# Performance work log

Hardware: AMD Instinct MI355X
Metric: run time of the kernel (lower is better)

## Reference

```python
import jax, jax.numpy as jnp
import numpy as np

DEPTH = 4
HEADS = 8
DIM = 512
DH = DIM // HEADS          # 64
M_FEAT = 256               # FAVOR+ random features
FF = 4 * DIM               # 2048
EPS_K = 1e-4               # FAVOR+ stabilizer
LN_EPS = 1e-5


def _gorf(rng, m, d):
    # gaussian orthogonal random features (lucidrains default, scaling=0)
    blocks = []
    for _ in range(m // d):
        g = rng.normal(size=(d, d))
        q, _ = np.linalg.qr(g)
        blocks.append(q.T)
    Q = np.concatenate(blocks, axis=0)[:m]
    mult = np.linalg.norm(rng.normal(size=(m, d)), axis=1)
    return (mult[:, None] * Q).astype(np.float32)


def setup_inputs() -> dict:
    rng = np.random.default_rng(0)
    B, T, L = 2, 8, 512
    s = 0.02
    x = rng.normal(size=(B, T, L, DIM)).astype(np.float32)
    proj = np.stack([_gorf(rng, M_FEAT, DH) for _ in range(DEPTH)])  # [depth, m, dh]
    def w(*shape):
        return (rng.normal(size=shape) * s).astype(np.float32)
    inp = {
        "x": jnp.asarray(x),
        "proj": jnp.asarray(proj),
        "ln1_g": jnp.ones((DEPTH, DIM), jnp.float32),
        "ln1_b": jnp.zeros((DEPTH, DIM), jnp.float32),
        "Wqkv": jnp.asarray(w(DEPTH, DIM, 3 * DIM)),
        "bqkv": jnp.zeros((DEPTH, 3 * DIM), jnp.float32),
        "Wo": jnp.asarray(w(DEPTH, DIM, DIM)),
        "bo": jnp.zeros((DEPTH, DIM), jnp.float32),
        "ln2_g": jnp.ones((DEPTH, DIM), jnp.float32),
        "ln2_b": jnp.zeros((DEPTH, DIM), jnp.float32),
        "Wff1": jnp.asarray(w(DEPTH, DIM, FF)),
        "bff1": jnp.zeros((DEPTH, FF), jnp.float32),
        "Wff2": jnp.asarray(w(DEPTH, FF, DIM)),
        "bff2": jnp.zeros((DEPTH, DIM), jnp.float32),
    }
    return inp


def _layer_norm(x, g, b):
    mu = jnp.mean(x, -1, keepdims=True)
    var = jnp.mean(jnp.square(x - mu), -1, keepdims=True)
    return (x - mu) * jax.lax.rsqrt(var + LN_EPS) * g + b


def _softmax_kernel(data, proj, is_query):
    # FAVOR+ positive softmax-kernel features (Performer)
    dh = data.shape[-1]
    dn = dh ** -0.25                       # data normalizer
    ratio = proj.shape[0] ** -0.5
    dd = jnp.einsum("bhnd,md->bhnm", data, proj) * dn
    diag = jnp.sum(jnp.square(data), -1, keepdims=True) * (0.5 * dn * dn)
    if is_query:
        mx = jnp.max(dd, axis=-1, keepdims=True)
    else:
        mx = jnp.max(dd, axis=(-1, -2), keepdims=True)
    return ratio * (jnp.exp(dd - diag - mx) + EPS_K)


def _attention(x, Wqkv, bqkv, Wo, bo, proj):
    B, N, D = x.shape
    qkv = x @ Wqkv + bqkv                                   # [B,N,3D]
    q, k, v = jnp.split(qkv, 3, axis=-1)
    def heads(t):
        return t.reshape(B, N, HEADS, DH).transpose(0, 2, 1, 3)  # [B,H,N,dh]
    q, k, v = heads(q), heads(k), heads(v)
    qp = _softmax_kernel(q, proj, True)                     # [B,H,N,m]
    kp = _softmax_kernel(k, proj, False)
    k_sum = jnp.sum(kp, axis=-2)                            # [B,H,m]
    d_inv = 1.0 / jnp.einsum("bhnm,bhm->bhn", qp, k_sum)
    ctx = jnp.einsum("bhnm,bhnd->bhmd", kp, v)              # [B,H,m,dh]
    out = jnp.einsum("bhmd,bhnm,bhn->bhnd", ctx, qp, d_inv)
    out = out.transpose(0, 2, 1, 3).reshape(B, N, D)
    return out @ Wo + bo


def reference(x, proj, ln1_g, ln1_b, Wqkv, bqkv, Wo, bo, ln2_g, ln2_b, Wff1, bff1, Wff2, bff2):
    B, T, L, D = x.shape
    h = x.reshape(B, T * L, D)
    for i in range(DEPTH):
        a = _attention(_layer_norm(h, ln1_g[i], ln1_b[i]), Wqkv[i], bqkv[i], Wo[i], bo[i], proj[i])
        h = h + a
        f = _layer_norm(h, ln2_g[i], ln2_b[i])
        f = jax.nn.gelu(f @ Wff1[i] + bff1[i], approximate=False) @ Wff2[i] + bff2[i]
        h = h + f
    return h.reshape(B, T, L, D)
```

## Files before the change

kernel.cpp:

```cpp
#include <hip/hip_runtime.h>
#include <math.h>

#define DEPTH 4
#define DMODEL 512
#define DH 64
#define MF 256
#define FFD 2048
#define SEQN 4096
#define NROWS 8192

typedef __bf16 bf16_t;
typedef bf16_t bf16x8 __attribute__((ext_vector_type(8)));
typedef bf16_t bf16x4 __attribute__((ext_vector_type(4)));
typedef bf16_t bf16x2 __attribute__((ext_vector_type(2)));
typedef float f32x4v __attribute__((ext_vector_type(4)));

static constexpr float DN = 0.35355339059327373f;
static constexpr float RATIO = 0.0625f;
static constexpr float EPSK = 1e-4f;

__device__ __forceinline__ float gelu_fast(float x) {
    float z2 = x * (1.5957691216f + 0.0713548162f * x * x);
    return x / (1.0f + __expf(-z2));
}

#define AS1(p) ((const __attribute__((address_space(1))) void*)(p))
#define AS3(p) ((__attribute__((address_space(3))) void*)(p))

template <int N> __device__ __forceinline__ void wait_vmcnt() {
    if constexpr (N == 0) asm volatile("s_waitcnt vmcnt(0)" ::: "memory");
    else if constexpr (N == 1) asm volatile("s_waitcnt vmcnt(1)" ::: "memory");
    else if constexpr (N == 2) asm volatile("s_waitcnt vmcnt(2)" ::: "memory");
    else if constexpr (N == 3) asm volatile("s_waitcnt vmcnt(3)" ::: "memory");
    else if constexpr (N == 4) asm volatile("s_waitcnt vmcnt(4)" ::: "memory");
    else if constexpr (N == 5) asm volatile("s_waitcnt vmcnt(5)" ::: "memory");
    else if constexpr (N == 6) asm volatile("s_waitcnt vmcnt(6)" ::: "memory");
    else if constexpr (N == 8) asm volatile("s_waitcnt vmcnt(8)" ::: "memory");
    else asm volatile("s_waitcnt vmcnt(12)" ::: "memory");
}

__global__ __launch_bounds__(256) void ln_kernel(const float* __restrict__ h,
                                                 const float* __restrict__ g,
                                                 const float* __restrict__ b,
                                                 bf16_t* __restrict__ y) {
    int row = blockIdx.x, tid = threadIdx.x;
    const float* hr = h + (size_t)row * DMODEL;
    float v0 = hr[tid], v1 = hr[tid + 256];
    __shared__ float s_sum[256], s_sq[256];
    s_sum[tid] = v0 + v1;
    s_sq[tid] = v0 * v0 + v1 * v1;
    __syncthreads();
    for (int off = 128; off > 0; off >>= 1) {
        if (tid < off) { s_sum[tid] += s_sum[tid + off]; s_sq[tid] += s_sq[tid + off]; }
        __syncthreads();
    }
    float mu = s_sum[0] * (1.0f / DMODEL);
    float var = s_sq[0] * (1.0f / DMODEL) - mu * mu;
    float rstd = rsqrtf(var + 1e-5f);
    bf16_t* yr = y + (size_t)row * DMODEL;
    yr[tid]       = (bf16_t)((v0 - mu) * rstd * g[tid] + b[tid]);
    yr[tid + 256] = (bf16_t)((v1 - mu) * rstd * g[tid + 256] + b[tid + 256]);
}

__global__ __launch_bounds__(256) void ln_add_kernel(const float* __restrict__ hin,
                                                     float* __restrict__ hout,
                                                     const bf16_t* __restrict__ p,
                                                     const float* __restrict__ g,
                                                     const float* __restrict__ b,
                                                     bf16_t* __restrict__ y) {
    int row = blockIdx.x, tid = threadIdx.x;
    const float* hr = hin + (size_t)row * DMODEL;
    const bf16_t* pr = p + (size_t)row * DMODEL;
    float2 hv = *(const float2*)(hr + 2 * tid);
    bf16x2 pv = *(const bf16x2*)(pr + 2 * tid);
    float v0 = hv.x + (float)pv[0];
    float v1 = hv.y + (float)pv[1];
    float2 outv; outv.x = v0; outv.y = v1;
    *(float2*)(hout + (size_t)row * DMODEL + 2 * tid) = outv;
    __shared__ float s_sum[256], s_sq[256];
    s_sum[tid] = v0 + v1;
    s_sq[tid] = v0 * v0 + v1 * v1;
    __syncthreads();
    for (int off = 128; off > 0; off >>= 1) {
        if (tid < off) { s_sum[tid] += s_sum[tid + off]; s_sq[tid] += s_sq[tid + off]; }
        __syncthreads();
    }
    float mu = s_sum[0] * (1.0f / DMODEL);
    float var = s_sq[0] * (1.0f / DMODEL) - mu * mu;
    float rstd = rsqrtf(var + 1e-5f);
    bf16x2 ov;
    ov[0] = (bf16_t)((v0 - mu) * rstd * g[2 * tid] + b[2 * tid]);
    ov[1] = (bf16_t)((v1 - mu) * rstd * g[2 * tid + 1] + b[2 * tid + 1]);
    *(bf16x2*)(y + (size_t)row * DMODEL + 2 * tid) = ov;
}

__global__ __launch_bounds__(256) void add_kernel(float* __restrict__ h,
                                                  const bf16_t* __restrict__ p) {
    size_t i = ((size_t)blockIdx.x * 256 + threadIdx.x) * 4;
    float4 hv = *(const float4*)(h + i);
    bf16x4 pv = *(const bf16x4*)(p + i);
    hv.x += (float)pv[0]; hv.y += (float)pv[1];
    hv.z += (float)pv[2]; hv.w += (float)pv[3];
    *(float4*)(h + i) = hv;
}

__global__ __launch_bounds__(256) void wconv_all(const float* __restrict__ Wqkv,
                                                 const float* __restrict__ Wo,
                                                 const float* __restrict__ Wff1,
                                                 const float* __restrict__ Wff2,
                                                 bf16_t* __restrict__ wslot) {
    __shared__ float t[32][33];
    int layer = blockIdx.y;
    int bid = blockIdx.x;
    const float* W; bf16_t* Wt; int K, N, nx, lb;
    bf16_t* slot = wslot + (size_t)layer * 3407872;
    if (bid < 768)       { W = Wqkv + (size_t)layer * 786432;  Wt = slot;           K = 512;  N = 1536; nx = 48; lb = bid; }
    else if (bid < 1024) { W = Wo   + (size_t)layer * 262144;  Wt = slot + 786432;  K = 512;  N = 512;  nx = 16; lb = bid - 768; }
    else if (bid < 2048) { W = Wff1 + (size_t)layer * 1048576; Wt = slot + 1048576; K = 512;  N = 2048; nx = 64; lb = bid - 1024; }
    else                 { W = Wff2 + (size_t)layer * 1048576; Wt = slot + 2097152; K = 2048; N = 512;  nx = 16; lb = bid - 2048; }
    int n0 = (lb % nx) * 32, k0 = (lb / nx) * 32;
    int tx = threadIdx.x & 31, ty = threadIdx.x >> 5;
#pragma unroll
    for (int i = 0; i < 32; i += 8)
        t[ty + i][tx] = W[(size_t)(k0 + ty + i) * N + n0 + tx];
    __syncthreads();
#pragma unroll
    for (int i = 0; i < 32; i += 8)
        Wt[(size_t)(n0 + ty + i) * K + k0 + tx] = (bf16_t)t[tx][ty + i];
}

__global__ __launch_bounds__(256) void pconv_kernel(const float* __restrict__ proj,
                                                    bf16_t* __restrict__ projb) {
    int i = (blockIdx.x * 256 + threadIdx.x) * 4;
    float4 v = *(const float4*)(proj + i);
    bf16x4 o;
    o[0] = (bf16_t)v.x; o[1] = (bf16_t)v.y; o[2] = (bf16_t)v.z; o[3] = (bf16_t)v.w;
    *(bf16x4*)(projb + i) = o;
}

template <int BM, int BN, int BK, int P, int ACT, int RES, int WF, int WB, int QKVE>
__global__ __launch_bounds__(256) void gemm_pipe(const bf16_t* __restrict__ A,
                                                 const bf16_t* __restrict__ Bt,
                                                 const float* __restrict__ bias,
                                                 float* __restrict__ Cf,
                                                 bf16_t* __restrict__ Cb,
                                                 bf16_t* __restrict__ Vt,
                                                 int N, int K) {
    static_assert(BK == 32, "BK fixed at 32 (KS==1)");
    constexpr int MR = BM / 2 / 16;
    constexpr int NR = BN / 2 / 16;
    constexpr int CH = BK / 8;
    constexpr int SWZ = CH - 1;
    constexpr int TILE = (BM + BN) * BK;
    constexpr int L = TILE / 8 / 256;
    __shared__ __attribute__((aligned(16))) bf16_t smem[P * TILE];
    int tid = threadIdx.x;
    int wv = tid >> 6, ln = tid & 63;
    int gx = gridDim.x;
    int lin = blockIdx.y * gx + blockIdx.x;
    int per = (gx * gridDim.y) >> 3;
    int orig = (lin & 7) * per + (lin >> 3);
    int m0 = (orig / gx) * BM, n0 = (orig % gx) * BN;
    int wr = (wv >> 1) * (MR * 16), wc = (wv & 1) * (NR * 16);
    int lr = ln & 15, kq8 = ln >> 4;
    int nsteps = K / BK;

    const bf16_t* gsrc[L];
    int ldst[L];
#pragma unroll
    for (int i = 0; i < L; i++) {
        int c = i * 256 + tid;
        int cb = i * 256 + (tid & ~63);
        bool inA = (c < BM * CH);
        int cc = inA ? c : c - BM * CH;
        int row = cc / CH, ch = cc % CH;
        const bf16_t* mat = inA ? A : Bt;
        int r0 = inA ? m0 : n0;
        int chs = ch ^ ((row ^ (row >> 2)) & SWZ);
        gsrc[i] = mat + (size_t)(r0 + row) * K + chs * 8;
        ldst[i] = cb * 8;
    }
    auto stage = [&](int tile, int sb) {
        int k0 = tile * BK;
        bf16_t* dst = smem + sb * TILE;
#pragma unroll
        for (int i = 0; i < L; i++)
            __builtin_amdgcn_global_load_lds(AS1(gsrc[i] + k0), AS3(dst + ldst[i]), 16, 0, 0);
    };

    int aoff[MR], boff[NR];
#pragma unroll
    for (int m = 0; m < MR; m++) {
        int row = wr + m * 16 + lr;
        aoff[m] = (row * CH + (kq8 ^ ((row ^ (row >> 2)) & SWZ))) * 8;
    }
#pragma unroll
    for (int n = 0; n < NR; n++) {
        int row = wc + n * 16 + lr;
        boff[n] = BM * BK + (row * CH + (kq8 ^ ((row ^ (row >> 2)) & SWZ))) * 8;
    }

    f32x4v acc[MR][NR] = {};
#pragma unroll
    for (int p = 0; p < P - 1; ++p) stage(p, p);

    int cur = 0;
    for (int t = 0; t < nsteps; ++t) {
        int rem = nsteps - 1 - t;
        if (rem >= P - 2) wait_vmcnt<(P - 2) * L>();
        else if constexpr (P >= 4) {
            if (rem == 1) wait_vmcnt<L>(); else wait_vmcnt<0>();
        } else wait_vmcnt<0>();
        __builtin_amdgcn_s_barrier();
        asm volatile("" ::: "memory");
        if (t + P - 1 < nsteps) {
            int sb = cur - 1; if (sb < 0) sb = P - 1;
            stage(t + P - 1, sb);
        }
        const bf16_t* base = smem + cur * TILE;
        bf16x8 af[MR], bfr[NR];
#pragma unroll
        for (int m = 0; m < MR; m++) af[m] = *(const bf16x8*)&base[aoff[m]];
#pragma unroll
        for (int n = 0; n < NR; n++) bfr[n] = *(const bf16x8*)&base[boff[n]];
        __builtin_amdgcn_s_setprio(1);
#pragma unroll
        for (int m = 0; m < MR; m++)
#pragma unroll
            for (int n = 0; n < NR; n++)
                acc[m][n] = __builtin_amdgcn_mfma_f32_16x16x32_bf16(af[m], bfr[n], acc[m][n], 0, 0, 0);
        __builtin_amdgcn_s_setprio(0);
        cur = (cur + 1 == P) ? 0 : cur + 1;
    }
    int rq = (ln >> 4) * 4;
    if (WB || QKVE) {
        __syncthreads();
        bf16_t* T = smem;
        constexpr int S = BN + 8;
#pragma unroll
        for (int n = 0; n < NR; n++) {
            int col = wc + n * 16 + lr;
            float bcol = bias[n0 + col];
#pragma unroll
            for (int m = 0; m < MR; m++) {
#pragma unroll
                for (int r = 0; r < 4; r++) {
                    int row = wr + m * 16 + rq + r;
                    float v = acc[m][n][r] + bcol;
                    if (ACT == 1) v = gelu_fast(v);
                    int cs = (col & 7) | ((((col >> 3) ^ (row >> 3)) & (BN / 8 - 1)) << 3);
                    T[row * S + cs] = (bf16_t)v;
                }
            }
        }
        __syncthreads();
        if (!QKVE || n0 < 1024) {
            int ldc = QKVE ? 1024 : N;
#pragma unroll
            for (int i = 0; i < BM * BN / 8 / 256; i++) {
                int e = i * 2048 + tid * 8;
                int row = e / BN, c0 = e % BN;
                int ch = ((c0 >> 3) ^ (row >> 3)) & (BN / 8 - 1);
                bf16x8 v = *(const bf16x8*)&T[row * S + ch * 8];
                *(bf16x8*)&Cb[(size_t)(m0 + row) * ldc + n0 + c0] = v;
            }
        } else {
#pragma unroll
            for (int i = 0; i < BM * BN / 8 / 256; i++) {
                int u = i * 256 + tid;
                int d = u & (BN - 1), nb8 = (u / BN) * 8;
                bf16x8 v;
#pragma unroll
                for (int j = 0; j < 8; j++) {
                    int row = nb8 + j;
                    int cs = (d & 7) | ((((d >> 3) ^ (row >> 3)) & (BN / 8 - 1)) << 3);
                    v[j] = T[row * S + cs];
                }
                int gcol = n0 + d;
                int hh2 = (gcol >> 6) & 7, dd2 = gcol & 63;
                int grow = m0 + nb8;
                int bb = grow >> 12, nn = grow & 4095;
                *(bf16x8*)&Vt[(((size_t)bb * 8 + hh2) * 64 + dd2) * 4096 + nn] = v;
            }
        }
    } else {
#pragma unroll
        for (int n = 0; n < NR; n++) {
            int col = n0 + wc + n * 16 + lr;
            float bcol = bias[col];
#pragma unroll
            for (int m = 0; m < MR; m++) {
#pragma unroll
                for (int r = 0; r < 4; r++) {
                    int row = m0 + wr + m * 16 + rq + r;
                    float v = acc[m][n][r] + bcol;
                    if (ACT == 1) v = gelu_fast(v);
                    size_t idx = (size_t)row * N + col;
                    if (RES) Cf[idx] += v;
                    else Cf[idx] = v;
                }
            }
        }
    }
}

__global__ __launch_bounds__(256) void feat_kernel(const bf16_t* __restrict__ qkvb,
                                                   const bf16_t* __restrict__ projb,
                                                   bf16_t* __restrict__ outp,
                                                   float* __restrict__ ksum_part) {
    int bid = blockIdx.x;
    int bh = bid >> 5, tile = bid & 31;
    int b = bh >> 3, hh = bh & 7;
    int tid = threadIdx.x, wv = tid >> 6, ln = tid & 63;
    __shared__ __attribute__((aligned(16))) bf16_t AsBs[128 * 64 + 256 * 64];
    bf16_t* As = AsBs;
    bf16_t* Bs = AsBs + 128 * 64;
    __shared__ float diag_s[128];
    __shared__ float ksp_s[256];
    int n0 = tile * 128;
    int qoff = 512 + hh * 64;
    int lrow8 = ln >> 3;
    int lchunk = ((ln & 7) ^ (lrow8 & 7)) * 8;
#pragma unroll
    for (int i = 0; i < 4; i++) {
        int e = wv * 4 + i;
        size_t src = (size_t)(b * SEQN + n0 + e * 8 + lrow8) * 1024 + qoff + lchunk;
        __builtin_amdgcn_global_load_lds(AS1(qkvb + src), AS3(&As[e * 512]), 16, 0, 0);
    }
#pragma unroll
    for (int i = 0; i < 8; i++) {
        int e = wv * 8 + i;
        size_t src = (size_t)(e * 8 + lrow8) * 64 + lchunk;
        __builtin_amdgcn_global_load_lds(AS1(projb + src), AS3(&Bs[e * 512]), 16, 0, 0);
    }
    __syncthreads();
    if (tid < 128) {
        float s = 0.f;
#pragma unroll
        for (int c = 0; c < 8; c++) {
            bf16x8 v = *(const bf16x8*)&As[tid * 64 + ((c ^ (tid & 7)) * 8)];
#pragma unroll
            for (int j = 0; j < 8; j++) { float f = (float)v[j]; s += f * f; }
        }
        diag_s[tid] = s * (0.5f * DN * DN);
    }
    int wr = (wv >> 1) * 64, wc = (wv & 1) * 128;
    int lr = ln & 15, kg = ln >> 4, rq = kg * 4;
    f32x4v acc[4][8] = {};
#pragma unroll
    for (int ks = 0; ks < 2; ks++) {
        int g = ks * 4 + kg;
        bf16x8 af[4], bfv[8];
#pragma unroll
        for (int m = 0; m < 4; m++) {
            int row = wr + m * 16 + lr;
            af[m] = *(const bf16x8*)&As[row * 64 + ((g ^ (row & 7)) * 8)];
        }
#pragma unroll
        for (int n = 0; n < 8; n++) {
            int row = wc + n * 16 + lr;
            bfv[n] = *(const bf16x8*)&Bs[row * 64 + ((g ^ (row & 7)) * 8)];
        }
#pragma unroll
        for (int m = 0; m < 4; m++)
#pragma unroll
            for (int n = 0; n < 8; n++)
                acc[m][n] = __builtin_amdgcn_mfma_f32_16x16x32_bf16(af[m], bfv[n], acc[m][n], 0, 0, 0);
    }
    __syncthreads();
    float sj[8] = {};
#pragma unroll
    for (int m = 0; m < 4; m++) {
#pragma unroll
        for (int n = 0; n < 8; n++) {
#pragma unroll
            for (int r = 0; r < 4; r++) {
                int row = wr + m * 16 + rq + r;
                float val = RATIO * (__expf(acc[m][n][r] * DN - diag_s[row]) + EPSK);
                acc[m][n][r] = val;
                sj[n] += val;
            }
        }
    }
#pragma unroll
    for (int n = 0; n < 8; n++) {
        sj[n] += __shfl_xor(sj[n], 16);
        sj[n] += __shfl_xor(sj[n], 32);
    }
    if (wv < 2 && ln < 16) {
#pragma unroll
        for (int n = 0; n < 8; n++) ksp_s[wc + n * 16 + ln] = sj[n];
    }
    __syncthreads();
    if (wv >= 2 && ln < 16) {
#pragma unroll
        for (int n = 0; n < 8; n++) ksp_s[wc + n * 16 + ln] += sj[n];
    }
    __syncthreads();
    ksum_part[(size_t)bid * 256 + tid] = ksp_s[tid];
    bf16_t* T = AsBs;
#pragma unroll
    for (int hf = 0; hf < 2; hf++) {
        if ((wv & 1) == hf) {
#pragma unroll
            for (int n = 0; n < 8; n++) {
                int mm = n * 16 + lr;
#pragma unroll
                for (int m = 0; m < 4; m++) {
                    int nnb = wr + m * 16 + rq;
                    bf16x4 v;
#pragma unroll
                    for (int r = 0; r < 4; r++) v[r] = (bf16_t)acc[m][n][r];
                    *(bf16x4*)&T[mm * 136 + nnb] = v;
                }
            }
        }
        __syncthreads();
#pragma unroll
        for (int i = 0; i < 8; i++) {
            int u = i * 256 + tid;
            int mm = u >> 4, nc = u & 15;
            bf16x8 v = *(const bf16x8*)&T[mm * 136 + nc * 8];
            *(bf16x8*)&outp[((size_t)bh * MF + hf * 128 + mm) * 4096 + n0 + nc * 8] = v;
        }
        __syncthreads();
    }
}

__global__ __launch_bounds__(256) void ctx_gemm(const bf16_t* __restrict__ KPt,
                                                const bf16_t* __restrict__ Vt,
                                                float* __restrict__ part) {
    int bh = blockIdx.y;
    int mtile = blockIdx.x & 1, kc = blockIdx.x >> 1;
    int m0 = mtile * 128, nb = kc * 512;
    int tid = threadIdx.x, wv = tid >> 6, ln = tid & 63;
    __shared__ __attribute__((aligned(16))) bf16_t As[128 * 64];
    __shared__ __attribute__((aligned(16))) bf16_t Bs[64 * 64];
    int lrow8 = ln >> 3;
    int lchunk = ((ln & 7) ^ (lrow8 & 7)) * 8;
    int lr = ln & 15, kg = ln >> 4, rq = kg * 4;
    int wr = wv * 32;
    f32x4v acc[2][4] = {};
    for (int kt = 0; kt < 8; kt++) {
        int noff = nb + kt * 64;
        __syncthreads();
#pragma unroll
        for (int i = 0; i < 4; i++) {
            int e = wv * 4 + i;
            __builtin_amdgcn_global_load_lds(
                AS1(KPt + ((size_t)bh * MF + m0 + e * 8 + lrow8) * 4096 + noff + lchunk),
                AS3(&As[e * 512]), 16, 0, 0);
        }
#pragma unroll
        for (int i = 0; i < 2; i++) {
            int e = wv * 2 + i;
            __builtin_amdgcn_global_load_lds(
                AS1(Vt + ((size_t)bh * 64 + e * 8 + lrow8) * 4096 + noff + lchunk),
                AS3(&Bs[e * 512]), 16, 0, 0);
        }
        __syncthreads();
#pragma unroll
        for (int ks = 0; ks < 2; ks++) {
            int g = ks * 4 + kg;
            bf16x8 af[2], bfv[4];
#pragma unroll
            for (int m = 0; m < 2; m++) {
                int row = wr + m * 16 + lr;
                af[m] = *(const bf16x8*)&As[row * 64 + ((g ^ (row & 7)) * 8)];
            }
#pragma unroll
            for (int n = 0; n < 4; n++) {
                int row = n * 16 + lr;
                bfv[n] = *(const bf16x8*)&Bs[row * 64 + ((g ^ (row & 7)) * 8)];
            }
#pragma unroll
            for (int m = 0; m < 2; m++)
#pragma unroll
                for (int n = 0; n < 4; n++)
                    acc[m][n] = __builtin_amdgcn_mfma_f32_16x16x32_bf16(af[m], bfv[n], acc[m][n], 0, 0, 0);
        }
    }
#pragma unroll
    for (int m = 0; m < 2; m++)
#pragma unroll
        for (int n = 0; n < 4; n++)
#pragma unroll
            for (int r = 0; r < 4; r++)
                part[((size_t)(kc * 16 + bh) * MF + m0 + wr + m * 16 + rq + r) * 64 + n * 16 + lr] =
                    acc[m][n][r];
}

__global__ __launch_bounds__(256) void ctx_reduce_kernel(const float* __restrict__ part,
                                                         const float* __restrict__ ksum_part,
                                                         bf16_t* __restrict__ ctx_t,
                                                         float* __restrict__ ksum) {
    int bh = blockIdx.x >> 4;
    int chunk = blockIdx.x & 15;
    for (int it = 0; it < 4; it++) {
        int idx = (chunk * 4 + it) * 256 + threadIdx.x;
        int m = idx >> 6, d = idx & 63;
        float s = 0.f;
#pragma unroll
        for (int kc = 0; kc < 8; kc++)
            s += part[(size_t)(kc * 16 + bh) * 16384 + idx];
        ctx_t[((size_t)bh * 64 + d) * MF + m] = (bf16_t)s;
    }
    if (chunk == 0) {
        float s = 0.f;
#pragma unroll
        for (int t = 0; t < 32; t++)
            s += ksum_part[((size_t)bh * 32 + t) * 256 + threadIdx.x];
        ksum[bh * MF + threadIdx.x] = s;
    }
}

__global__ __launch_bounds__(256) void qfused_kernel(const bf16_t* __restrict__ qkvb,
                                                     const bf16_t* __restrict__ projb,
                                                     const bf16_t* __restrict__ ctx_t,
                                                     const float* __restrict__ ksumb,
                                                     bf16_t* __restrict__ abuf) {
    int bid = blockIdx.x;
    int bh = bid >> 5, tile = bid & 31;
    int b = bh >> 3, hh = bh & 7;
    int tid = threadIdx.x, wv = tid >> 6, ln = tid & 63;
    __shared__ __attribute__((aligned(16))) bf16_t Qs[128 * 64];
    __shared__ __attribute__((aligned(16))) bf16_t Ps[256 * 64];
    __shared__ __attribute__((aligned(16))) bf16_t Cs[64 * 256];
    __shared__ float diag_s[128];
    __shared__ float dsum_s[128];
    int n0 = tile * 128;
    int lrow8 = ln >> 3;
    int lchunk = ((ln & 7) ^ (lrow8 & 7)) * 8;
#pragma unroll
    for (int i = 0; i < 4; i++) {
        int e = wv * 4 + i;
        size_t src = (size_t)(b * SEQN + n0 + e * 8 + lrow8) * 1024 + hh * 64 + lchunk;
        __builtin_amdgcn_global_load_lds(AS1(qkvb + src), AS3(&Qs[e * 512]), 16, 0, 0);
    }
#pragma unroll
    for (int i = 0; i < 8; i++) {
        int e = wv * 8 + i;
        size_t src = (size_t)(e * 8 + lrow8) * 64 + lchunk;
        __builtin_amdgcn_global_load_lds(AS1(projb + src), AS3(&Ps[e * 512]), 16, 0, 0);
    }
#pragma unroll
    for (int i = 0; i < 8; i++) {
        int c = i * 256 + tid;
        int cb = i * 256 + (tid & ~63);
        int crow = c >> 5, cch = c & 31;
        size_t src = ((size_t)bh * 64 + crow) * 256 + (size_t)(cch ^ (crow & 7)) * 8;
        __builtin_amdgcn_global_load_lds(AS1(ctx_t + src), AS3(Cs + (size_t)cb * 8), 16, 0, 0);
    }
    int wr = (wv >> 1) * 64, wc = (wv & 1) * 128;
    int lr = ln & 15, kg = ln >> 4, rq = kg * 4;
    float ksum_r[8];
#pragma unroll
    for (int n = 0; n < 8; n++) ksum_r[n] = ksumb[bh * MF + wc + n * 16 + lr];
    __syncthreads();
    if (tid < 128) {
        float s = 0.f;
#pragma unroll
        for (int c = 0; c < 8; c++) {
            bf16x8 v = *(const bf16x8*)&Qs[tid * 64 + ((c ^ (tid & 7)) * 8)];
#pragma unroll
            for (int j = 0; j < 8; j++) { float f = (float)v[j]; s += f * f; }
        }
        diag_s[tid] = s * (0.5f * DN * DN);
    }
    f32x4v acc[4][8] = {};
#pragma unroll
    for (int ks = 0; ks < 2; ks++) {
        int g = ks * 4 + kg;
        bf16x8 af[4], bfv[8];
#pragma unroll
        for (int m = 0; m < 4; m++) {
            int row = wr + m * 16 + lr;
            af[m] = *(const bf16x8*)&Qs[row * 64 + ((g ^ (row & 7)) * 8)];
        }
#pragma unroll
        for (int n = 0; n < 8; n++) {
            int row = wc + n * 16 + lr;
            bfv[n] = *(const bf16x8*)&Ps[row * 64 + ((g ^ (row & 7)) * 8)];
        }
#pragma unroll
        for (int m = 0; m < 4; m++)
#pragma unroll
            for (int n = 0; n < 8; n++)
                acc[m][n] = __builtin_amdgcn_mfma_f32_16x16x32_bf16(af[m], bfv[n], acc[m][n], 0, 0, 0);
    }
    __syncthreads();
    float dsum_p[4][4];
#pragma unroll
    for (int m = 0; m < 4; m++) {
#pragma unroll
        for (int r = 0; r < 4; r++) {
            int row = wr + m * 16 + rq + r;
            float dg = diag_s[row];
            float ds = 0.f;
#pragma unroll
            for (int n = 0; n < 8; n++) {
                float val = RATIO * (__expf(acc[m][n][r] * DN - dg) + EPSK);
                acc[m][n][r] = val;
                ds += val * ksum_r[n];
            }
            dsum_p[m][r] = ds;
        }
    }
#pragma unroll
    for (int m = 0; m < 4; m++)
#pragma unroll
        for (int r = 0; r < 4; r++) {
#pragma unroll
            for (int mask = 1; mask < 16; mask <<= 1)
                dsum_p[m][r] += __shfl_xor(dsum_p[m][r], mask);
        }
    if ((wv & 1) == 0 && lr == 0) {
#pragma unroll
        for (int m = 0; m < 4; m++)
#pragma unroll
            for (int r = 0; r < 4; r++)
                dsum_s[wr + m * 16 + rq + r] = dsum_p[m][r];
    }
    __syncthreads();
    if ((wv & 1) == 1 && lr == 0) {
#pragma unroll
        for (int m = 0; m < 4; m++)
#pragma unroll
            for (int r = 0; r < 4; r++) {
                int row = wr + m * 16 + rq + r;
                dsum_s[row] = 1.0f / (dsum_s[row] + dsum_p[m][r]);
            }
    }
    __syncthreads();
    f32x4v acc_o[4][2] = {};
#pragma unroll
    for (int h = 0; h < 2; h++) {
        if ((wv & 1) == h) {
#pragma unroll
            for (int m = 0; m < 4; m++)
#pragma unroll
                for (int n = 0; n < 8; n++)
#pragma unroll
                    for (int r = 0; r < 4; r++) {
                        int row = wr + m * 16 + rq + r;
                        int ml = n * 16 + lr;
                        Ps[row * 128 + (((ml >> 3) ^ (row & 7)) * 8) + (ml & 7)] =
                            (bf16_t)acc[m][n][r];
                    }
        }
        __syncthreads();
#pragma unroll
        for (int ku = 0; ku < 4; ku++) {
            int g = ku * 4 + kg;
            bf16x8 af[4], bfv[2];
#pragma unroll
            for (int m = 0; m < 4; m++) {
                int row = wr + m * 16 + lr;
                af[m] = *(const bf16x8*)&Ps[row * 128 + ((g ^ (row & 7)) * 8)];
            }
#pragma unroll
            for (int n = 0; n < 2; n++) {
                int rowd = (wv & 1) * 32 + n * 16 + lr;
                int ch = (h * 16 + g) ^ (rowd & 7);
                bfv[n] = *(const bf16x8*)&Cs[(rowd * 32 + ch) * 8];
            }
#pragma unroll
            for (int m = 0; m < 4; m++)
#pragma unroll
                for (int n = 0; n < 2; n++)
                    acc_o[m][n] = __builtin_amdgcn_mfma_f32_16x16x32_bf16(af[m], bfv[n], acc_o[m][n], 0, 0, 0);
        }
        __syncthreads();
    }
#pragma unroll
    for (int m = 0; m < 4; m++) {
#pragma unroll
        for (int r = 0; r < 4; r++) {
            int rowl = wr + m * 16 + rq + r;
            float di = dsum_s[rowl];
            size_t obase = ((size_t)(b * SEQN + n0 + rowl)) * DMODEL + hh * 64;
#pragma unroll
            for (int n = 0; n < 2; n++) {
                int d = (wv & 1) * 32 + n * 16 + lr;
                abuf[obase + d] = (bf16_t)(acc_o[m][n][r] * di);
            }
        }
    }
}

extern "C" void kernel_launch(void* const* d_in, const int* in_sizes, int n_in,
                              void* d_out, int out_size, void* d_ws, size_t ws_size,
                              hipStream_t stream) {
    const float* x     = (const float*)d_in[0];
    const float* proj  = (const float*)d_in[1];
    const float* ln1_g = (const float*)d_in[2];
    const float* ln1_b = (const float*)d_in[3];
    const float* Wqkv  = (const float*)d_in[4];
    const float* bqkv  = (const float*)d_in[5];
    const float* Wo    = (const float*)d_in[6];
    const float* bo    = (const float*)d_in[7];
    const float* ln2_g = (const float*)d_in[8];
    const float* ln2_b = (const float*)d_in[9];
    const float* Wff1  = (const float*)d_in[10];
    const float* bff1  = (const float*)d_in[11];
    const float* Wff2  = (const float*)d_in[12];
    const float* bff2  = (const float*)d_in[13];

    float* h = (float*)d_out;
    char* ws = (char*)d_ws;
    bf16_t* KPt   = (bf16_t*)(ws);
    bf16_t* ybf   = (bf16_t*)(ws);
    bf16_t* pWo   = (bf16_t*)(ws + 8388608);
    bf16_t* pFF2  = (bf16_t*)(ws + 16777216);
    bf16_t* qkvb  = (bf16_t*)(ws + 33554432);
    bf16_t* abufb = (bf16_t*)(ws + 50331648);
    float*  ctx_part  = (float*)(ws + 58720256);
    float*  ksum_part = (float*)(ws + 67108864);
    bf16_t* ffmidb    = (bf16_t*)(ws + 50331648);
    bf16_t* Vt    = (bf16_t*)(ws + 83886080);
    bf16_t* projb = (bf16_t*)(ws + 92274688);
    bf16_t* ctx_t = (bf16_t*)(ws + 92405760);
    float*  ksumb = (float*)(ws + 92930048);
    bf16_t* wbase = (bf16_t*)(ws + 93061120);
    const size_t WSLOT = 3407872;
    bool hoist = ws_size >= (size_t)93061120 + 4 * 6815744;

    pconv_kernel<<<64, 256, 0, stream>>>(proj, projb);
    if (hoist)
        wconv_all<<<dim3(3072, 4), 256, 0, stream>>>(Wqkv, Wo, Wff1, Wff2, wbase);

    for (int i = 0; i < DEPTH; i++) {
        const bf16_t* pj = projb + (size_t)i * MF * DH;
        if (!hoist)
            wconv_all<<<dim3(3072, 1), 256, 0, stream>>>(
                Wqkv + (size_t)i * 786432, Wo + (size_t)i * 262144,
                Wff1 + (size_t)i * 1048576, Wff2 + (size_t)i * 1048576, wbase);
        bf16_t* wl = wbase + (hoist ? (size_t)i * WSLOT : 0);
        bf16_t* wq_t = wl;
        bf16_t* wo_t = wl + 786432;
        bf16_t* w1_t = wl + 1048576;
        bf16_t* w2_t = wl + 2097152;

        if (i == 0)
            ln_kernel<<<NROWS, 256, 0, stream>>>(x, ln1_g, ln1_b, ybf);
        else
            ln_add_kernel<<<NROWS, 256, 0, stream>>>(h, h, pFF2, ln1_g + i * DMODEL,
                                                     ln1_b + i * DMODEL, ybf);
        gemm_pipe<128, 64, 32, 3, 0, 0, 0, 0, 1>
            <<<dim3(1536 / 64, NROWS / 128), 256, 0, stream>>>(
            ybf, wq_t, bqkv + i * 1536, nullptr, qkvb, Vt, 1536, 512);
        feat_kernel<<<512, 256, 0, stream>>>(qkvb, pj, KPt, ksum_part);
        ctx_gemm<<<dim3(16, 16), 256, 0, stream>>>(KPt, Vt, ctx_part);
        ctx_reduce_kernel<<<256, 256, 0, stream>>>(ctx_part, ksum_part, ctx_t, ksumb);
        qfused_kernel<<<512, 256, 0, stream>>>(qkvb, pj, ctx_t, ksumb, abufb);
        gemm_pipe<128, 64, 32, 3, 0, 0, 0, 1, 0>
            <<<dim3(512 / 64, NROWS / 128), 256, 0, stream>>>(
            abufb, wo_t, bo + i * DMODEL, nullptr, pWo, nullptr, 512, 512);

        ln_add_kernel<<<NROWS, 256, 0, stream>>>(i == 0 ? x : h, h, pWo,
                                                 ln2_g + i * DMODEL,
                                                 ln2_b + i * DMODEL, ybf);
        gemm_pipe<128, 64, 32, 3, 1, 0, 0, 1, 0>
            <<<dim3(2048 / 64, NROWS / 128), 256, 0, stream>>>(
            ybf, w1_t, bff1 + i * FFD, nullptr, ffmidb, nullptr, 2048, 512);
        gemm_pipe<128, 64, 32, 3, 0, 0, 0, 1, 0>
            <<<dim3(512 / 64, NROWS / 128), 256, 0, stream>>>(
            ffmidb, w2_t, bff2 + i * DMODEL, nullptr, pFF2, nullptr, 512, 2048);
    }
    add_kernel<<<4096, 256, 0, stream>>>(h, pFF2);
}
```

Before: 717.3 us.

## Fuse key-feature context GEMM into feat_kernel, dropping the KPt round trip

feat_kernel now also loads the matching 128-row V tile into shared memory and multiplies the in-LDS key features by V with MFMA, writing per-tile fp32 partial contexts directly. This removes the ctx_gemm launch and the global write and re-read of the bf16 KPt feature matrix. In exchange, ctx_reduce must sum 32 partials instead of 8, the partial buffer grows to 32 slices, and feat_kernel uses extra LDS, which may lower occupancy. The workspace layout is shifted to fit the larger partial buffer.

Measured after the change: 694.6 us. -3.2%, faster.

```diff
diff --git a/kernel.cpp b/kernel.cpp
--- a/kernel.cpp
+++ b/kernel.cpp
@@ -306,13 +306,15 @@
 
 __global__ __launch_bounds__(256) void feat_kernel(const bf16_t* __restrict__ qkvb,
                                                    const bf16_t* __restrict__ projb,
-                                                   bf16_t* __restrict__ outp,
+                                                   const bf16_t* __restrict__ Vt,
+                                                   float* __restrict__ ctx_part,
                                                    float* __restrict__ ksum_part) {
     int bid = blockIdx.x;
     int bh = bid >> 5, tile = bid & 31;
     int b = bh >> 3, hh = bh & 7;
     int tid = threadIdx.x, wv = tid >> 6, ln = tid & 63;
     __shared__ __attribute__((aligned(16))) bf16_t AsBs[128 * 64 + 256 * 64];
+    __shared__ __attribute__((aligned(16))) bf16_t Vs[64 * 128];
     bf16_t* As = AsBs;
     bf16_t* Bs = AsBs + 128 * 64;
     __shared__ float diag_s[128];
@@ -333,6 +335,15 @@
         size_t src = (size_t)(e * 8 + lrow8) * 64 + lchunk;
         __builtin_amdgcn_global_load_lds(AS1(projb + src), AS3(&Bs[e * 512]), 16, 0, 0);
     }
+#pragma unroll
+    for (int i = 0; i < 4; i++) {
+        int c = i * 256 + tid;
+        int cb = i * 256 + (tid & ~63);
+        int row = c >> 4, ch = c & 15;
+        int chs = ch ^ (row & 15);
+        size_t src = (size_t)(bh * 64 + row) * 4096 + n0 + chs * 8;
+        __builtin_amdgcn_global_load_lds(AS1(Vt + src), AS3(&Vs[cb * 8]), 16, 0, 0);
+    }
     __syncthreads();
     if (tid < 128) {
         float s = 0.f;
@@ -399,6 +410,7 @@
     __syncthreads();
     ksum_part[(size_t)bid * 256 + tid] = ksp_s[tid];
     bf16_t* T = AsBs;
+    float* cpb = ctx_part + (size_t)(tile * 16 + bh) * 16384;
 #pragma unroll
     for (int hf = 0; hf < 2; hf++) {
         if ((wv & 1) == hf) {
@@ -416,78 +428,39 @@
             }
         }
         __syncthreads();
-#pragma unroll
-        for (int i = 0; i < 8; i++) {
-            int u = i * 256 + tid;
-            int mm = u >> 4, nc = u & 15;
-            bf16x8 v = *(const bf16x8*)&T[mm * 136 + nc * 8];
-            *(bf16x8*)&outp[((size_t)bh * MF + hf * 128 + mm) * 4096 + n0 + nc * 8] = v;
+        f32x4v accp[2][4] = {};
+#pragma unroll
+        for (int ks = 0; ks < 4; ks++) {
+            int g = ks * 4 + kg;
+            bf16x8 apv[2], bpv[4];
+#pragma unroll
+            for (int mt = 0; mt < 2; mt++) {
+                int rowm = (wv * 2 + mt) * 16 + lr;
+                apv[mt] = *(const bf16x8*)&T[rowm * 136 + g * 8];
+            }
+#pragma unroll
+            for (int dt = 0; dt < 4; dt++) {
+                int d = dt * 16 + lr;
+                bpv[dt] = *(const bf16x8*)&Vs[d * 128 + ((g ^ (d & 15)) * 8)];
+            }
+#pragma unroll
+            for (int mt = 0; mt < 2; mt++)
+#pragma unroll
+                for (int dt = 0; dt < 4; dt++)
+                    accp[mt][dt] = __builtin_amdgcn_mfma_f32_16x16x32_bf16(apv[mt], bpv[dt], accp[mt][dt], 0, 0, 0);
+        }
+#pragma unroll
+        for (int mt = 0; mt < 2; mt++) {
+#pragma unroll
+            for (int r = 0; r < 4; r++) {
+                int mfeat = hf * 128 + (wv * 2 + mt) * 16 + rq + r;
+#pragma unroll
+                for (int dt = 0; dt < 4; dt++)
+                    cpb[(size_t)mfeat * 64 + dt * 16 + lr] = accp[mt][dt][r];
+            }
         }
         __syncthreads();
     }
-}
-
-__global__ __launch_bounds__(256) void ctx_gemm(const bf16_t* __restrict__ KPt,
-                                                const bf16_t* __restrict__ Vt,
-                                                float* __restrict__ part) {
-    int bh = blockIdx.y;
-    int mtile = blockIdx.x & 1, kc = blockIdx.x >> 1;
-    int m0 = mtile * 128, nb = kc * 512;
-    int tid = threadIdx.x, wv = tid >> 6, ln = tid & 63;
-    __shared__ __attribute__((aligned(16))) bf16_t As[128 * 64];
-    __shared__ __attribute__((aligned(16))) bf16_t Bs[64 * 64];
-    int lrow8 = ln >> 3;
-    int lchunk = ((ln & 7) ^ (lrow8 & 7)) * 8;
-    int lr = ln & 15, kg = ln >> 4, rq = kg * 4;
-    int wr = wv * 32;
-    f32x4v acc[2][4] = {};
-    for (int kt = 0; kt < 8; kt++) {
-        int noff = nb + kt * 64;
-        __syncthreads();
-#pragma unroll
-        for (int i = 0; i < 4; i++) {
-            int e = wv * 4 + i;
-            __builtin_amdgcn_global_load_lds(
-                AS1(KPt + ((size_t)bh * MF + m0 + e * 8 + lrow8) * 4096 + noff + lchunk),
-                AS3(&As[e * 512]), 16, 0, 0);
-        }
-#pragma unroll
-        for (int i = 0; i < 2; i++) {
-            int e = wv * 2 + i;
-            __builtin_amdgcn_global_load_lds(
-                AS1(Vt + ((size_t)bh * 64 + e * 8 + lrow8) * 4096 + noff + lchunk),
-                AS3(&Bs[e * 512]), 16, 0, 0);
-        }
-        __syncthreads();
-#pragma unroll
-        for (int ks = 0; ks < 2; ks++) {
-            int g = ks * 4 + kg;
-            bf16x8 af[2], bfv[4];
-#pragma unroll
-            for (int m = 0; m < 2; m++) {
-                int row = wr + m * 16 + lr;
-                af[m] = *(const bf16x8*)&As[row * 64 + ((g ^ (row & 7)) * 8)];
-            }
-#pragma unroll
-            for (int n = 0; n < 4; n++) {
-                int row = n * 16 + lr;
-                bfv[n] = *(const bf16x8*)&Bs[row * 64 + ((g ^ (row & 7)) * 8)];
-            }
-#pragma unroll
-            for (int m = 0; m < 2; m++)
-#pragma unroll
-                for (int n = 0; n < 4; n++)
-                    acc[m][n] = __builtin_amdgcn_mfma_f32_16x16x32_bf16(af[m], bfv[n], acc[m][n], 0, 0, 0);
-        }
-    }
-#pragma unroll
-    for (int m = 0; m < 2; m++)
-#pragma unroll
-        for (int n = 0; n < 4; n++)
-#pragma unroll
-            for (int r = 0; r < 4; r++)
-                part[((size_t)(kc * 16 + bh) * MF + m0 + wr + m * 16 + rq + r) * 64 + n * 16 + lr] =
-                    acc[m][n][r];
 }
 
 __global__ __launch_bounds__(256) void ctx_reduce_kernel(const float* __restrict__ part,
@@ -501,7 +474,7 @@
         int m = idx >> 6, d = idx & 63;
         float s = 0.f;
 #pragma unroll
-        for (int kc = 0; kc < 8; kc++)
+        for (int kc = 0; kc < 32; kc++)
             s += part[(size_t)(kc * 16 + bh) * 16384 + idx];
         ctx_t[((size_t)bh * 64 + d) * MF + m] = (bf16_t)s;
     }
@@ -708,22 +681,21 @@
 
     float* h = (float*)d_out;
     char* ws = (char*)d_ws;
-    bf16_t* KPt   = (bf16_t*)(ws);
     bf16_t* ybf   = (bf16_t*)(ws);
     bf16_t* pWo   = (bf16_t*)(ws + 8388608);
     bf16_t* pFF2  = (bf16_t*)(ws + 16777216);
     bf16_t* qkvb  = (bf16_t*)(ws + 33554432);
     bf16_t* abufb = (bf16_t*)(ws + 50331648);
-    float*  ctx_part  = (float*)(ws + 58720256);
-    float*  ksum_part = (float*)(ws + 67108864);
-    bf16_t* ffmidb    = (bf16_t*)(ws + 50331648);
-    bf16_t* Vt    = (bf16_t*)(ws + 83886080);
-    bf16_t* projb = (bf16_t*)(ws + 92274688);
-    bf16_t* ctx_t = (bf16_t*)(ws + 92405760);
-    float*  ksumb = (float*)(ws + 92930048);
-    bf16_t* wbase = (bf16_t*)(ws + 93061120);
+    float*  ctx_part = (float*)(ws + 58720256);
+    bf16_t* ffmidb   = (bf16_t*)(ws + 50331648);
+    bf16_t* Vt    = (bf16_t*)(ws + 92274688);
+    bf16_t* projb = (bf16_t*)(ws + 100663296);
+    bf16_t* ctx_t = (bf16_t*)(ws + 100794368);
+    float*  ksumb = (float*)(ws + 101318656);
+    float*  ksum_part = (float*)(ws + 101335040);
+    bf16_t* wbase = (bf16_t*)(ws + 101859328);
     const size_t WSLOT = 3407872;
-    bool hoist = ws_size >= (size_t)93061120 + 4 * 6815744;
+    bool hoist = ws_size >= (size_t)101859328 + 4 * 6815744;
 
     pconv_kernel<<<64, 256, 0, stream>>>(proj, projb);
     if (hoist)
@@ -749,8 +721,7 @@
         gemm_pipe<128, 64, 32, 3, 0, 0, 0, 0, 1>
             <<<dim3(1536 / 64, NROWS / 128), 256, 0, stream>>>(
             ybf, wq_t, bqkv + i * 1536, nullptr, qkvb, Vt, 1536, 512);
-        feat_kernel<<<512, 256, 0, stream>>>(qkvb, pj, KPt, ksum_part);
-        ctx_gemm<<<dim3(16, 16), 256, 0, stream>>>(KPt, Vt, ctx_part);
+        feat_kernel<<<512, 256, 0, stream>>>(qkvb, pj, Vt, ctx_part, ksum_part);
         ctx_reduce_kernel<<<256, 256, 0, stream>>>(ctx_part, ksum_part, ctx_t, ksumb);
         qfused_kernel<<<512, 256, 0, stream>>>(qkvb, pj, ctx_t, ksumb, abufb);
         gemm_pipe<128, 64, 32, 3, 0, 0, 0, 1, 0>
```
